# Performance work log

Measured on AMD Instinct MI355X. Metric: run time of the kernel, lower is better.

The kernel has to match this reference:

```python
import jax, jax.numpy as jnp
import numpy as np

EPS = 1e-12
NR_ITERS = 8


def _sqrt_newton_raphson(S):
    # iterative sqrt approximation, faithful to the torch module
    x = jnp.where(S > 1.0, S * 0.5, jnp.ones_like(S))
    for _ in range(NR_ITERS):
        x = 0.5 * (x + S / (x + 1e-09))
    return x


def setup_inputs() -> dict:
    key = jax.random.key(0)
    ks = jax.random.split(key, 8)
    B, S, H, V, P, T = 64, 512, 768, 30522, 512, 2
    return {
        "input_ids": jax.random.randint(ks[0], (B, S), 0, V, dtype=jnp.int32),
        "token_type_ids": jax.random.randint(ks[1], (B, S), 0, T, dtype=jnp.int32),
        "word_table": jax.random.randint(ks[2], (V, H), 0, 127, dtype=jnp.int32),
        "word_scale": jax.random.uniform(ks[3], (1,), dtype=jnp.float32) * 0.01 + 0.001,
        "pos_table": jax.random.randint(ks[4], (P, H), 0, 127, dtype=jnp.int32),
        "pos_scale": jax.random.uniform(ks[5], (1,), dtype=jnp.float32) * 0.01 + 0.001,
        "type_table": jax.random.randint(ks[6], (T, H), 0, 127, dtype=jnp.int32),
        "type_scale": jax.random.uniform(ks[7], (1,), dtype=jnp.float32) * 0.01 + 0.001,
        "ln_weight": jax.random.uniform(jax.random.fold_in(key, 10), (H,), dtype=jnp.float32) + 0.5,
        "ln_bias": jax.random.normal(jax.random.fold_in(key, 11), (H,), dtype=jnp.float32) * 0.02,
    }


def reference(input_ids, token_type_ids, word_table, word_scale, pos_table,
              pos_scale, type_table, type_scale, ln_weight, ln_bias):
    B, S = input_ids.shape
    pos_ids = jnp.arange(S, dtype=jnp.int32)  # broadcast over batch

    # int8-style gather + per-tensor dequant
    word_emb = word_table[input_ids].astype(jnp.float32) * word_scale
    pos_emb = pos_table[pos_ids].astype(jnp.float32) * pos_scale  # [S,H] broadcasts
    type_emb = type_table[token_type_ids].astype(jnp.float32) * type_scale
    emb = word_emb + pos_emb[None, :, :] + type_emb  # [B,S,H]

    # approximate LayerNorm with Newton-Raphson sqrt
    mean = emb.mean(axis=-1, keepdims=True)
    var = jnp.mean(jnp.square(emb - mean), axis=-1, keepdims=True)  # unbiased=False
    std_approx = _sqrt_newton_raphson(var)
    normed = (emb - mean) / (std_approx + EPS)
    # dropout is identity at inference
    return ln_weight * normed + ln_bias
```

## Files before the change

### kernel.cpp

```cpp
#include <hip/hip_runtime.h>


constexpr int H_DIM = 768;
constexpr int TPB = 256;
constexpr int TOK_PER_BLK = 4;

typedef float nfloat4 __attribute__((ext_vector_type(4)));

__global__ __launch_bounds__(TPB) void bert_emb_kernel(
    const int* __restrict__ input_ids,
    const int* __restrict__ token_type_ids,
    const int* __restrict__ word_table,
    const float* __restrict__ word_scale,
    const int* __restrict__ pos_table,
    const float* __restrict__ pos_scale,
    const int* __restrict__ type_table,
    const float* __restrict__ type_scale,
    const float* __restrict__ ln_w,
    const float* __restrict__ ln_b,
    float* __restrict__ out,
    int n_tokens, int S)
{
    const int wave = threadIdx.x >> 6;
    const int lane = threadIdx.x & 63;
    const int token = blockIdx.x * TOK_PER_BLK + wave;
    if (token >= n_tokens) return;

    const int s   = token % S;
    const int wid = input_ids[token];
    const int tt  = token_type_ids[token];

    const float ws = word_scale[0];
    const float ps = pos_scale[0];
    const float ts = type_scale[0];

    const int4* __restrict__ wrow = (const int4*)(word_table + (long long)wid * H_DIM);
    const int4* __restrict__ prow = (const int4*)(pos_table  + (long long)s   * H_DIM);
    const int4* __restrict__ trow = (const int4*)(type_table + (long long)tt  * H_DIM);

    float e[3][4];
    float sum = 0.f;
    float sq  = 0.f;
#pragma unroll
    for (int j = 0; j < 3; ++j) {
        const int g = j * 64 + lane;
        const int4 w4 = wrow[g];
        const int4 p4 = prow[g];
        const int4 t4 = trow[g];
        e[j][0] = (float)w4.x * ws + (float)p4.x * ps + (float)t4.x * ts;
        e[j][1] = (float)w4.y * ws + (float)p4.y * ps + (float)t4.y * ts;
        e[j][2] = (float)w4.z * ws + (float)p4.z * ps + (float)t4.z * ts;
        e[j][3] = (float)w4.w * ws + (float)p4.w * ps + (float)t4.w * ts;
#pragma unroll
        for (int k = 0; k < 4; ++k) {
            sum += e[j][k];
            sq  += e[j][k] * e[j][k];
        }
    }

#pragma unroll
    for (int off = 1; off < 64; off <<= 1) {
        sum += __shfl_xor(sum, off);
        sq  += __shfl_xor(sq, off);
    }
    const float mean = sum * (1.0f / (float)H_DIM);
    float var = sq * (1.0f / (float)H_DIM) - mean * mean;
    var = var < 0.f ? 0.f : var;

    const float inv = 1.0f / (sqrtf(var) + 1e-12f);

    nfloat4* __restrict__ orow = (nfloat4*)(out + (long long)token * H_DIM);
    const float4* __restrict__ lwv = (const float4*)ln_w;
    const float4* __restrict__ lbv = (const float4*)ln_b;
#pragma unroll
    for (int j = 0; j < 3; ++j) {
        const int g = j * 64 + lane;
        const float4 lw = lwv[g];
        const float4 lb = lbv[g];
        nfloat4 o;
        o.x = lw.x * ((e[j][0] - mean) * inv) + lb.x;
        o.y = lw.y * ((e[j][1] - mean) * inv) + lb.y;
        o.z = lw.z * ((e[j][2] - mean) * inv) + lb.z;
        o.w = lw.w * ((e[j][3] - mean) * inv) + lb.w;
        __builtin_nontemporal_store(o, &orow[g]);
    }
}

extern "C" void kernel_launch(void* const* d_in, const int* in_sizes, int n_in,
                              void* d_out, int out_size, void* d_ws, size_t ws_size,
                              hipStream_t stream) {
    const int*   input_ids      = (const int*)d_in[0];
    const int*   token_type_ids = (const int*)d_in[1];
    const int*   word_table     = (const int*)d_in[2];
    const float* word_scale     = (const float*)d_in[3];
    const int*   pos_table      = (const int*)d_in[4];
    const float* pos_scale      = (const float*)d_in[5];
    const int*   type_table     = (const int*)d_in[6];
    const float* type_scale     = (const float*)d_in[7];
    const float* ln_w           = (const float*)d_in[8];
    const float* ln_b           = (const float*)d_in[9];
    float* out = (float*)d_out;

    const int n_tokens = in_sizes[0];
    const int S = in_sizes[4] / H_DIM;

    const int blocks = (n_tokens + TOK_PER_BLK - 1) / TOK_PER_BLK;
    bert_emb_kernel<<<blocks, TPB, 0, stream>>>(
        input_ids, token_type_ids, word_table, word_scale,
        pos_table, pos_scale, type_table, type_scale,
        ln_w, ln_b, out, n_tokens, S);
}
```

Measured before the change: 200.3 us.

## Use persistent grid-stride waves with double-buffered row prefetch

```diff
diff --git a/kernel.cpp b/kernel.cpp
--- a/kernel.cpp
+++ b/kernel.cpp
@@ -2,12 +2,72 @@
 
 
 constexpr int H_DIM = 768;
-constexpr int TPB = 256;
-constexpr int TOK_PER_BLK = 4;
+constexpr int TPB   = 256;
+constexpr int WPB   = TPB / 64;
+constexpr int NBLK  = 2048;
 
 typedef float nfloat4 __attribute__((ext_vector_type(4)));
 
-__global__ __launch_bounds__(TPB) void bert_emb_kernel(
+struct RowBuf { int4 w[3], p[3], t[3]; };
+
+__device__ __forceinline__ void issue_rows(
+    RowBuf& b, int wid, int s, int ty, int lane,
+    const int* __restrict__ word_table,
+    const int* __restrict__ pos_table,
+    const int* __restrict__ type_table)
+{
+    const int4* __restrict__ wr = (const int4*)(word_table + (size_t)wid * H_DIM);
+    const int4* __restrict__ pr = (const int4*)(pos_table  + (size_t)s   * H_DIM);
+    const int4* __restrict__ tr = (const int4*)(type_table + (size_t)ty  * H_DIM);
+#pragma unroll
+    for (int j = 0; j < 3; ++j) {
+        const int g = j * 64 + lane;
+        b.w[j] = wr[g];
+        b.p[j] = pr[g];
+        b.t[j] = tr[g];
+    }
+}
+
+__device__ __forceinline__ void finish_token(
+    const RowBuf& b, int token, int lane,
+    float ws, float ps, float ts,
+    const float4 lw[3], const float4 lb[3],
+    float* __restrict__ out)
+{
+    float e[3][4];
+    float sum = 0.f, sq = 0.f;
+#pragma unroll
+    for (int j = 0; j < 3; ++j) {
+        e[j][0] = (float)b.w[j].x * ws + (float)b.p[j].x * ps + (float)b.t[j].x * ts;
+        e[j][1] = (float)b.w[j].y * ws + (float)b.p[j].y * ps + (float)b.t[j].y * ts;
+        e[j][2] = (float)b.w[j].z * ws + (float)b.p[j].z * ps + (float)b.t[j].z * ts;
+        e[j][3] = (float)b.w[j].w * ws + (float)b.p[j].w * ps + (float)b.t[j].w * ts;
+#pragma unroll
+        for (int k = 0; k < 4; ++k) { sum += e[j][k]; sq += e[j][k] * e[j][k]; }
+    }
+#pragma unroll
+    for (int off = 1; off < 64; off <<= 1) {
+        sum += __shfl_xor(sum, off);
+        sq  += __shfl_xor(sq, off);
+    }
+    const float mean = sum * (1.0f / (float)H_DIM);
+    float var = sq * (1.0f / (float)H_DIM) - mean * mean;
+    var = var < 0.f ? 0.f : var;
+    const float inv = 1.0f / (sqrtf(var) + 1e-12f);
+
+    nfloat4* __restrict__ orow = (nfloat4*)(out + (size_t)token * H_DIM);
+#pragma unroll
+    for (int j = 0; j < 3; ++j) {
+        nfloat4 o;
+        o.x = lw[j].x * ((e[j][0] - mean) * inv) + lb[j].x;
+        o.y = lw[j].y * ((e[j][1] - mean) * inv) + lb[j].y;
+        o.z = lw[j].z * ((e[j][2] - mean) * inv) + lb[j].z;
+        o.w = lw[j].w * ((e[j][3] - mean) * inv) + lb[j].w;
+        __builtin_nontemporal_store(o, &orow[j * 64 + lane]);
+    }
+}
+
+__global__ __launch_bounds__(TPB, 4) void bert_emb_kernel(
     const int* __restrict__ input_ids,
     const int* __restrict__ token_type_ids,
     const int* __restrict__ word_table,
@@ -21,68 +81,45 @@
     float* __restrict__ out,
     int n_tokens, int S)
 {
-    const int wave = threadIdx.x >> 6;
-    const int lane = threadIdx.x & 63;
-    const int token = blockIdx.x * TOK_PER_BLK + wave;
-    if (token >= n_tokens) return;
+    const int wave  = threadIdx.x >> 6;
+    const int lane  = threadIdx.x & 63;
+    const int gwave = blockIdx.x * WPB + wave;
+    const int nwave = gridDim.x * WPB;
 
-    const int s   = token % S;
-    const int wid = input_ids[token];
-    const int tt  = token_type_ids[token];
+    int t = gwave;
+    if (t >= n_tokens) return;
 
     const float ws = word_scale[0];
     const float ps = pos_scale[0];
     const float ts = type_scale[0];
 
-    const int4* __restrict__ wrow = (const int4*)(word_table + (long long)wid * H_DIM);
-    const int4* __restrict__ prow = (const int4*)(pos_table  + (long long)s   * H_DIM);
-    const int4* __restrict__ trow = (const int4*)(type_table + (long long)tt  * H_DIM);
-
-    float e[3][4];
-    float sum = 0.f;
-    float sq  = 0.f;
+    float4 lw[3], lb[3];
 #pragma unroll
     for (int j = 0; j < 3; ++j) {
-        const int g = j * 64 + lane;
-        const int4 w4 = wrow[g];
-        const int4 p4 = prow[g];
-        const int4 t4 = trow[g];
-        e[j][0] = (float)w4.x * ws + (float)p4.x * ps + (float)t4.x * ts;
-        e[j][1] = (float)w4.y * ws + (float)p4.y * ps + (float)t4.y * ts;
-        e[j][2] = (float)w4.z * ws + (float)p4.z * ps + (float)t4.z * ts;
-        e[j][3] = (float)w4.w * ws + (float)p4.w * ps + (float)t4.w * ts;
-#pragma unroll
-        for (int k = 0; k < 4; ++k) {
-            sum += e[j][k];
-            sq  += e[j][k] * e[j][k];
-        }
+        lw[j] = ((const float4*)ln_w)[j * 64 + lane];
+        lb[j] = ((const float4*)ln_b)[j * 64 + lane];
     }
 
-#pragma unroll
-    for (int off = 1; off < 64; off <<= 1) {
-        sum += __shfl_xor(sum, off);
-        sq  += __shfl_xor(sq, off);
-    }
-    const float mean = sum * (1.0f / (float)H_DIM);
-    float var = sq * (1.0f / (float)H_DIM) - mean * mean;
-    var = var < 0.f ? 0.f : var;
+    RowBuf A, B;
+    issue_rows(A, input_ids[t], t % S, token_type_ids[t], lane,
+               word_table, pos_table, type_table);
 
-    const float inv = 1.0f / (sqrtf(var) + 1e-12f);
+    for (;;) {
+        int tn = t + nwave;
+        if (tn < n_tokens)
+            issue_rows(B, input_ids[tn], tn % S, token_type_ids[tn], lane,
+                       word_table, pos_table, type_table);
+        finish_token(A, t, lane, ws, ps, ts, lw, lb, out);
+        if (tn >= n_tokens) return;
+        t = tn;
 
-    nfloat4* __restrict__ orow = (nfloat4*)(out + (long long)token * H_DIM);
-    const float4* __restrict__ lwv = (const float4*)ln_w;
-    const float4* __restrict__ lbv = (const float4*)ln_b;
-#pragma unroll
-    for (int j = 0; j < 3; ++j) {
-        const int g = j * 64 + lane;
-        const float4 lw = lwv[g];
-        const float4 lb = lbv[g];
-        nfloat4 o;
-        o.x = lw.x * ((e[j][0] - mean) * inv) + lb.x;
-        o.y = lw.y * ((e[j][1] - mean) * inv) + lb.y;
-        o.z = lw.z * ((e[j][2] - mean) * inv) + lb.z;
-        o.w = lw.w * ((e[j][3] - mean) * inv) + lb.w;
-        __builtin_nontemporal_store(o, &orow[g]);
+        tn = t + nwave;
+        if (tn < n_tokens)
+            issue_rows(A, input_ids[tn], tn % S, token_type_ids[tn], lane,
+                       word_table, pos_table, type_table);
+        finish_token(B, t, lane, ws, ps, ts, lw, lb, out);
+        if (tn >= n_tokens) return;
+        t = tn;
     }
 }
 
@@ -104,7 +141,11 @@
     const int n_tokens = in_sizes[0];
     const int S = in_sizes[4] / H_DIM;
 
-    const int blocks = (n_tokens + TOK_PER_BLK - 1) / TOK_PER_BLK;
+    const int waves_needed  = (n_tokens + 0) ;
+    const int blocks_needed = (n_tokens + WPB - 1) / WPB;
+    const int blocks = blocks_needed < NBLK ? blocks_needed : NBLK;
+    (void)waves_needed;
+
     bert_emb_kernel<<<blocks, TPB, 0, stream>>>(
         input_ids, token_type_ids, word_table, word_scale,
         pos_table, pos_scale, type_table, type_scale,
```

Measured after the change: 240.4 us. 20.0% more time.
